# Kernel optimization log

Hardware: AMD Instinct MI355X
Metric: run time of the kernel (lower is better)

The kernel has to match this reference:

```python
import jax, jax.numpy as jnp
import numpy as np

D_MODEL = 1024
NUM_HEADS = 16
DEPTH = D_MODEL // NUM_HEADS
B, S = 4, 2048


def setup_inputs() -> dict:
    key = jax.random.key(0)
    ks = jax.random.split(key, 12)
    s = 1.0 / np.sqrt(D_MODEL)
    return {
        "q": jax.random.normal(ks[0], (B, S, D_MODEL), jnp.float32),
        "k": jax.random.normal(ks[1], (B, S, D_MODEL), jnp.float32),
        "v": jax.random.normal(ks[2], (B, S, D_MODEL), jnp.float32),
        "mask": jax.random.randint(ks[3], (B, S), 0, 2, jnp.int32),
        "wq_w": jax.random.uniform(ks[4], (D_MODEL, D_MODEL), jnp.float32, -s, s),
        "wq_b": jnp.zeros((D_MODEL,), jnp.float32),
        "wk_w": jax.random.uniform(ks[5], (D_MODEL, D_MODEL), jnp.float32, -s, s),
        "wk_b": jnp.zeros((D_MODEL,), jnp.float32),
        "wv_w": jax.random.uniform(ks[6], (D_MODEL, D_MODEL), jnp.float32, -s, s),
        "wv_b": jnp.zeros((D_MODEL,), jnp.float32),
        "wo_w": jax.random.uniform(ks[7], (D_MODEL, D_MODEL), jnp.float32, -s, s),
        "wo_b": jnp.zeros((D_MODEL,), jnp.float32),
    }


def _split_heads(x):
    # [B, S, D] -> [B, H, S, depth]
    b, s, _ = x.shape
    return x.reshape(b, s, NUM_HEADS, DEPTH).transpose(0, 2, 1, 3)


def reference(q, k, v, mask, wq_w, wq_b, wk_w, wk_b, wv_w, wv_b, wo_w, wo_b):
    qh = _split_heads(q @ wq_w.T + wq_b)
    kh = _split_heads(k @ wk_w.T + wk_b)
    vh = _split_heads(v @ wv_w.T + wv_b)
    # [B, H, Sq, Sk]
    logits = jnp.einsum("bhqd,bhkd->bhqk", qh, kh) / jnp.sqrt(
        jnp.asarray(DEPTH, jnp.float32))
    # 2D mask -> [B, 1, 1, Sk], masked_fill where mask == 0
    m = mask[:, None, None, :]
    logits = jnp.where(m == 0, jnp.asarray(-1e9, logits.dtype), logits)
    attn = jax.nn.softmax(logits, axis=-1)
    out = jnp.einsum("bhqk,bhkd->bhqd", attn, vh)
    out = out.transpose(0, 2, 1, 3).reshape(q.shape[0], -1, D_MODEL)
    return out @ wo_w.T + wo_b
```

## Files before the change

kernel.cpp:

```cpp
#include <hip/hip_runtime.h>
#include <hip/hip_bf16.h>
#include <stdint.h>

typedef __bf16 bf16_t;
typedef __bf16 bf16x8 __attribute__((ext_vector_type(8)));
typedef __bf16 bf16x2 __attribute__((ext_vector_type(2)));
typedef float  f32x4  __attribute__((ext_vector_type(4)));
typedef float  f32x16 __attribute__((ext_vector_type(16)));
typedef unsigned int u32;
typedef u32 u32x4 __attribute__((ext_vector_type(4)));

#define D_MODEL 1024
#define NHEAD   16
#define DEPTH   64
#define BATCH   4
#define SEQ     2048
#define MROWS   (BATCH*SEQ)

#define SC 0.18033688011112042f

__device__ __forceinline__ void gload16(const void* g, void* l) {
    __builtin_amdgcn_global_load_lds(
        (__attribute__((address_space(1))) void*)(uintptr_t)g,
        (__attribute__((address_space(3))) void*)l,
        16, 0, 0);
}

__device__ __forceinline__ u32 pk2(float a, float b) {
    bf16x2 t; t[0] = (bf16_t)a; t[1] = (bf16_t)b;
    return __builtin_bit_cast(u32, t);
}

__global__ __launch_bounds__(256) void cvt_kernel(const float* __restrict__ src,
                                                  bf16_t* __restrict__ dst, int n8) {
    int i = blockIdx.x * 256 + threadIdx.x;
    if (i >= n8) return;
    const float4* s4 = (const float4*)src;
    float4 a = s4[2*(size_t)i], b = s4[2*(size_t)i + 1];
    bf16x8 o;
    o[0] = (bf16_t)a.x; o[1] = (bf16_t)a.y; o[2] = (bf16_t)a.z; o[3] = (bf16_t)a.w;
    o[4] = (bf16_t)b.x; o[5] = (bf16_t)b.y; o[6] = (bf16_t)b.z; o[7] = (bf16_t)b.w;
    *(bf16x8*)(dst + 8*(size_t)i) = o;
}

__global__ __launch_bounds__(256) void vtrans_kernel(const bf16_t* __restrict__ Vp,
                                                     bf16_t* __restrict__ Vt) {
    __shared__ bf16_t T[64][257];
    const int bh = blockIdx.y;
    const int b = bh >> 4, h = bh & 15;
    const int s0 = blockIdx.x * 256;
    const int tid = threadIdx.x;
#pragma unroll
    for (int p = 0; p < 8; ++p) {
        int id = p*256 + tid;
        int sl = id >> 3, dg = id & 7;
        bf16x8 v = *(const bf16x8*)&Vp[((size_t)b*SEQ + s0 + sl)*D_MODEL + h*DEPTH + dg*8];
#pragma unroll
        for (int e = 0; e < 8; ++e) T[dg*8 + e][sl] = v[e];
    }
    __syncthreads();
#pragma unroll
    for (int p = 0; p < 8; ++p) {
        int id = p*256 + tid;
        int d = id >> 5, sg = id & 31;
        bf16x8 o;
#pragma unroll
        for (int e = 0; e < 8; ++e) {
            int sp = sg*8 + e;
            int s  = (sp & ~12) | ((sp & 4) << 1) | ((sp & 8) >> 1);
            o[e] = T[d][s];
        }
        *(bf16x8*)&Vt[((size_t)bh*DEPTH + d)*SEQ + s0 + sg*8] = o;
    }
}

template<int OUT_BF16>
__global__ __launch_bounds__(256) void gemm_bt(const bf16_t* __restrict__ A,
                                               const bf16_t* __restrict__ Bw,
                                               const float* __restrict__ bias,
                                               bf16_t* __restrict__ Cb,
                                               float* __restrict__ Cf,
                                               int M, int N, int K) {
    __shared__ bf16_t As[128*64];
    __shared__ bf16_t Bs[128*64];
    const int tid  = threadIdx.x;
    const int wave = tid >> 6, lane = tid & 63;
    const int lr = lane & 15, lk = (lane >> 4) * 8;
    const int bm = blockIdx.x * 128, bn = blockIdx.y * 128;
    const int wr = (wave >> 1) * 64, wc = (wave & 1) * 64;

    f32x4 acc[4][4] = {};

    for (int kt = 0; kt < K; kt += 64) {
#pragma unroll
        for (int p = 0; p < 4; ++p) {
            int chunk = p*256 + tid;
            int r  = chunk >> 3;
            int cs = ((chunk & 7) ^ (r & 7)) * 8;
            gload16(A  + (size_t)(bm + r)*K + kt + cs, As + (size_t)(p*256 + wave*64)*8);
            gload16(Bw + (size_t)(bn + r)*K + kt + cs, Bs + (size_t)(p*256 + wave*64)*8);
        }
        __syncthreads();
        const char* AsB = (const char*)As;
        const char* BsB = (const char*)Bs;
#pragma unroll
        for (int ks = 0; ks < 2; ++ks) {
            int kb = (ks*32 + lk) * 2;
            bf16x8 af[4], bfv[4];
#pragma unroll
            for (int mi = 0; mi < 4; ++mi) {
                int row = wr + mi*16 + lr;
                af[mi] = *(const bf16x8*)(AsB + ((row*128 + kb) ^ ((row & 7) << 4)));
            }
#pragma unroll
            for (int ni = 0; ni < 4; ++ni) {
                int row = wc + ni*16 + lr;
                bfv[ni] = *(const bf16x8*)(BsB + ((row*128 + kb) ^ ((row & 7) << 4)));
            }
            __builtin_amdgcn_s_setprio(1);
#pragma unroll
            for (int mi = 0; mi < 4; ++mi)
#pragma unroll
                for (int ni = 0; ni < 4; ++ni)
                    acc[mi][ni] = __builtin_amdgcn_mfma_f32_16x16x32_bf16(
                        af[mi], bfv[ni], acc[mi][ni], 0, 0, 0);
            __builtin_amdgcn_s_setprio(0);
        }
        __syncthreads();
    }

#pragma unroll
    for (int ni = 0; ni < 4; ++ni) {
        int col = bn + wc + ni*16 + lr;
        float bv = bias[col];
#pragma unroll
        for (int mi = 0; mi < 4; ++mi) {
#pragma unroll
            for (int j = 0; j < 4; ++j) {
                int row = bm + wr + mi*16 + (lane >> 4)*4 + j;
                float vv = acc[mi][ni][j] + bv;
                if (OUT_BF16) Cb[(size_t)row*N + col] = (bf16_t)vv;
                else          Cf[(size_t)row*N + col] = vv;
            }
        }
    }
}

__global__ __launch_bounds__(256) void attn_kernel(const bf16_t* __restrict__ Qp,
                                                   const bf16_t* __restrict__ Kp,
                                                   const bf16_t* __restrict__ Vt,
                                                   const int* __restrict__ mask,
                                                   bf16_t* __restrict__ AO) {
    __shared__ bf16_t Ks[2][64*64];
    __shared__ bf16_t Vs[2][64*64];
    __shared__ float  mb[2][64];

    const int tid  = threadIdx.x;
    const int wave = tid >> 6, lane = tid & 63;
    const int lr5 = lane & 31;
    const int hi  = lane >> 5;
    const int b = blockIdx.z, h = blockIdx.y, q0 = blockIdx.x * 128;
    const int qw = q0 + wave*32;
    const size_t base  = (size_t)b * SEQ * D_MODEL + (size_t)h * DEPTH;
    const size_t vbase = ((size_t)(b*NHEAD + h)) * DEPTH * SEQ;

    bf16x8 qf[4];
#pragma unroll
    for (int dc = 0; dc < 4; ++dc)
        qf[dc] = *(const bf16x8*)&Qp[base + (size_t)(qw + lr5)*D_MODEL + dc*16 + hi*8];

    f32x16 o0 = {}, o1 = {};
    float m_run = -1e30f, l_run = 0.f;

    {
#pragma unroll
        for (int p = 0; p < 2; ++p) {
            int chunk = p*256 + tid; int r = chunk >> 3;
            int cs = ((chunk & 7) ^ (r & 7)) * 8;
            gload16(Kp + base + (size_t)r*D_MODEL + cs, (bf16_t*)Ks[0] + (size_t)chunk*8);
            gload16(Vt + vbase + (size_t)r*SEQ + cs,   (bf16_t*)Vs[0] + (size_t)chunk*8);
        }
        if (tid < 64) mb[0][tid] = (mask[(size_t)b*SEQ + tid] == 0) ? -1e30f : 0.f;
    }
    __syncthreads();

    for (int t = 0; t < SEQ/64; ++t) {
        const int cur = t & 1, nxt = cur ^ 1;
        if (t + 1 < SEQ/64) {
#pragma unroll
            for (int p = 0; p < 2; ++p) {
                int chunk = p*256 + tid; int r = chunk >> 3;
                int cs = ((chunk & 7) ^ (r & 7)) * 8;
                gload16(Kp + base + (size_t)((t+1)*64 + r)*D_MODEL + cs,
                        (bf16_t*)Ks[nxt] + (size_t)chunk*8);
                gload16(Vt + vbase + (size_t)r*SEQ + (t+1)*64 + cs,
                        (bf16_t*)Vs[nxt] + (size_t)chunk*8);
            }
            if (tid < 64) mb[nxt][tid] = (mask[(size_t)b*SEQ + (t+1)*64 + tid] == 0) ? -1e30f : 0.f;
        }

        const char* KsB = (const char*)Ks[cur];
        f32x16 s0 = {}, s1 = {};
#pragma unroll
        for (int dc = 0; dc < 4; ++dc) {
            int colb = dc*32 + hi*16;
            int row0 = lr5, row1 = 32 + lr5;
            bf16x8 kf0 = *(const bf16x8*)(KsB + ((row0*128 + colb) ^ ((row0 & 7) << 4)));
            bf16x8 kf1 = *(const bf16x8*)(KsB + ((row1*128 + colb) ^ ((row1 & 7) << 4)));
            __builtin_amdgcn_s_setprio(1);
            s0 = __builtin_amdgcn_mfma_f32_32x32x16_bf16(kf0, qf[dc], s0, 0, 0, 0);
            s1 = __builtin_amdgcn_mfma_f32_32x32x16_bf16(kf1, qf[dc], s1, 0, 0, 0);
            __builtin_amdgcn_s_setprio(0);
        }

        const float* mbp = mb[cur];
        f32x4 mv[2][4];
#pragma unroll
        for (int kt = 0; kt < 2; ++kt)
#pragma unroll
            for (int g = 0; g < 4; ++g)
                mv[kt][g] = *(const f32x4*)&mbp[kt*32 + g*8 + hi*4];

        float pv[32];
#pragma unroll
        for (int r = 0; r < 16; ++r) {
            pv[r]      = s0[r]*SC + mv[0][r>>2][r&3];
            pv[16 + r] = s1[r]*SC + mv[1][r>>2][r&3];
        }

        float rmax = fmaxf(pv[0], pv[1]);
#pragma unroll
        for (int r = 2; r < 32; r += 2) rmax = fmaxf(fmaxf(pv[r], pv[r+1]), rmax);
        rmax = fmaxf(rmax, __shfl_xor(rmax, 32));

        if (!__all(rmax <= m_run + 8.f)) {
            float mn  = fmaxf(m_run, rmax);
            float fac = __builtin_exp2f(m_run - mn);
            m_run = mn;
            l_run *= fac;
#pragma unroll
            for (int r = 0; r < 16; ++r) { o0[r] *= fac; o1[r] *= fac; }
        }
        float sum = 0.f;
#pragma unroll
        for (int r = 0; r < 32; ++r) { pv[r] = __builtin_exp2f(pv[r] - m_run); sum += pv[r]; }
        sum += __shfl_xor(sum, 32);
        l_run += sum;

        const char* VsB = (const char*)Vs[cur];
#pragma unroll
        for (int kt = 0; kt < 2; ++kt) {
#pragma unroll
            for (int c = 0; c < 2; ++c) {
                u32x4 fwv;
#pragma unroll
                for (int i = 0; i < 4; ++i)
                    fwv[i] = pk2(pv[kt*16 + c*8 + 2*i], pv[kt*16 + c*8 + 2*i + 1]);
                bf16x8 pfrag = __builtin_bit_cast(bf16x8, fwv);
                int colb = kt*64 + c*32 + hi*16;
                int row0 = lr5, row1 = 32 + lr5;
                bf16x8 vf0 = *(const bf16x8*)(VsB + ((row0*128 + colb) ^ ((row0 & 7) << 4)));
                bf16x8 vf1 = *(const bf16x8*)(VsB + ((row1*128 + colb) ^ ((row1 & 7) << 4)));
                __builtin_amdgcn_s_setprio(1);
                o0 = __builtin_amdgcn_mfma_f32_32x32x16_bf16(vf0, pfrag, o0, 0, 0, 0);
                o1 = __builtin_amdgcn_mfma_f32_32x32x16_bf16(vf1, pfrag, o1, 0, 0, 0);
                __builtin_amdgcn_s_setprio(0);
            }
        }
        __syncthreads();
    }

    float inv = 1.f / l_run;
    char* TrB = (char*)Ks;
    const int qloc = wave*32 + lr5;
#pragma unroll
    for (int mt = 0; mt < 2; ++mt)
#pragma unroll
        for (int r = 0; r < 16; ++r) {
            int d = mt*32 + (r & 3) + 8*(r >> 2) + 4*hi;
            float val = (mt ? o1[r] : o0[r]) * inv;
            *(bf16_t*)(TrB + (qloc*128 + ((d*2) ^ ((qloc & 7) << 4)))) = (bf16_t)val;
        }
    __syncthreads();
#pragma unroll
    for (int p = 0; p < 4; ++p) {
        int id = p*256 + tid;
        int row = id >> 3, g = id & 7;
        bf16x8 v8 = *(const bf16x8*)(TrB + (row*128 + ((g*16) ^ ((row & 7) << 4))));
        *(bf16x8*)&AO[base + (size_t)(q0 + row)*D_MODEL + g*8] = v8;
    }
}

extern "C" void kernel_launch(void* const* d_in, const int* in_sizes, int n_in,
                              void* d_out, int out_size, void* d_ws, size_t ws_size,
                              hipStream_t stream) {
    (void)in_sizes; (void)n_in; (void)out_size; (void)ws_size;
    const float* q    = (const float*)d_in[0];
    const float* k    = (const float*)d_in[1];
    const float* v    = (const float*)d_in[2];
    const int*   mask = (const int*)d_in[3];
    const float* wq_w = (const float*)d_in[4];
    const float* wq_b = (const float*)d_in[5];
    const float* wk_w = (const float*)d_in[6];
    const float* wk_b = (const float*)d_in[7];
    const float* wv_w = (const float*)d_in[8];
    const float* wv_b = (const float*)d_in[9];
    const float* wo_w = (const float*)d_in[10];
    const float* wo_b = (const float*)d_in[11];
    float* out = (float*)d_out;

    const size_t ACT = (size_t)MROWS * D_MODEL;
    const size_t WSZ = (size_t)D_MODEL * D_MODEL;
    bf16_t* Xb = (bf16_t*)d_ws;
    bf16_t* Qp = Xb + ACT;
    bf16_t* Kp = Qp + ACT;
    bf16_t* Vp = Kp + ACT;
    bf16_t* Wq = Vp + ACT;
    bf16_t* Wk = Wq + WSZ;
    bf16_t* Wv = Wk + WSZ;
    bf16_t* Wo = Wv + WSZ;
    bf16_t* Vt = Xb;
    bf16_t* AO = Vp;

    const int wn8 = (int)(WSZ/8), an8 = (int)(ACT/8);
    cvt_kernel<<<dim3(wn8/256), dim3(256), 0, stream>>>(wq_w, Wq, wn8);
    cvt_kernel<<<dim3(wn8/256), dim3(256), 0, stream>>>(wk_w, Wk, wn8);
    cvt_kernel<<<dim3(wn8/256), dim3(256), 0, stream>>>(wv_w, Wv, wn8);
    cvt_kernel<<<dim3(wn8/256), dim3(256), 0, stream>>>(wo_w, Wo, wn8);

    dim3 ggrid(MROWS/128, D_MODEL/128);
    cvt_kernel<<<dim3(an8/256), dim3(256), 0, stream>>>(q, Xb, an8);
    gemm_bt<1><<<ggrid, dim3(256), 0, stream>>>(Xb, Wq, wq_b, Qp, nullptr, MROWS, D_MODEL, D_MODEL);
    cvt_kernel<<<dim3(an8/256), dim3(256), 0, stream>>>(k, Xb, an8);
    gemm_bt<1><<<ggrid, dim3(256), 0, stream>>>(Xb, Wk, wk_b, Kp, nullptr, MROWS, D_MODEL, D_MODEL);
    cvt_kernel<<<dim3(an8/256), dim3(256), 0, stream>>>(v, Xb, an8);
    gemm_bt<1><<<ggrid, dim3(256), 0, stream>>>(Xb, Wv, wv_b, Vp, nullptr, MROWS, D_MODEL, D_MODEL);

    vtrans_kernel<<<dim3(SEQ/256, NHEAD*BATCH), dim3(256), 0, stream>>>(Vp, Vt);

    attn_kernel<<<dim3(SEQ/128, NHEAD, BATCH), dim3(256), 0, stream>>>(Qp, Kp, Vt, mask, AO);

    gemm_bt<0><<<ggrid, dim3(256), 0, stream>>>(AO, Wo, wo_b, nullptr, out, MROWS, D_MODEL, D_MODEL);
}
```

Baseline: 285.4 us.

## Triple-buffer K/V tiles, preload mask bias once, and remap blocks across XCDs

Attention K/V staging moves from double to triple buffering, prefetching two tiles ahead. Each iteration waits with a partial vmcnt so loads can stay in flight across the barrier. The per-tile mask load is replaced by a single up-front conversion of the whole mask row into a bf16 bias array in shared memory. Blocks are remapped so each XCD handles consistent (batch, head) groups, which should improve L2 reuse of K/V. LDS usage rises, which may reduce occupancy, and the hand-written waitcnt depends on the exact count of outstanding loads.

```diff
diff --git a/kernel.cpp b/kernel.cpp
--- a/kernel.cpp
+++ b/kernel.cpp
@@ -4,6 +4,7 @@
 
 typedef __bf16 bf16_t;
 typedef __bf16 bf16x8 __attribute__((ext_vector_type(8)));
+typedef __bf16 bf16x4 __attribute__((ext_vector_type(4)));
 typedef __bf16 bf16x2 __attribute__((ext_vector_type(2)));
 typedef float  f32x4  __attribute__((ext_vector_type(4)));
 typedef float  f32x16 __attribute__((ext_vector_type(16)));
@@ -151,55 +152,73 @@
                                                    const bf16_t* __restrict__ Vt,
                                                    const int* __restrict__ mask,
                                                    bf16_t* __restrict__ AO) {
-    __shared__ bf16_t Ks[2][64*64];
-    __shared__ bf16_t Vs[2][64*64];
-    __shared__ float  mb[2][64];
+    __shared__ bf16_t Ks[3][64*64];
+    __shared__ bf16_t Vs[3][64*64];
+    __shared__ bf16_t mbias[SEQ];
 
     const int tid  = threadIdx.x;
     const int wave = tid >> 6, lane = tid & 63;
     const int lr5 = lane & 31;
     const int hi  = lane >> 5;
-    const int b = blockIdx.z, h = blockIdx.y, q0 = blockIdx.x * 128;
+
+    const int flat = blockIdx.x + 16*blockIdx.y + 256*blockIdx.z;
+    const int xcd = flat & 7, slot = flat >> 3;
+    const int bh = xcd + 8*(slot >> 4);
+    const int b = bh >> 4, h = bh & 15;
+    const int q0 = (slot & 15) * 128;
+
     const int qw = q0 + wave*32;
     const size_t base  = (size_t)b * SEQ * D_MODEL + (size_t)h * DEPTH;
-    const size_t vbase = ((size_t)(b*NHEAD + h)) * DEPTH * SEQ;
+    const size_t vbase = (size_t)bh * DEPTH * SEQ;
 
     bf16x8 qf[4];
 #pragma unroll
     for (int dc = 0; dc < 4; ++dc)
         qf[dc] = *(const bf16x8*)&Qp[base + (size_t)(qw + lr5)*D_MODEL + dc*16 + hi*8];
 
-    f32x16 o0 = {}, o1 = {};
-    float m_run = -1e30f, l_run = 0.f;
-
     {
+        const int4* mp = (const int4*)&mask[(size_t)b*SEQ + tid*8];
+        int4 m0 = mp[0], m1 = mp[1];
+        bf16x8 mm;
+        mm[0] = (m0.x == 0) ? (bf16_t)(-1e30f) : (bf16_t)0.0f;
+        mm[1] = (m0.y == 0) ? (bf16_t)(-1e30f) : (bf16_t)0.0f;
+        mm[2] = (m0.z == 0) ? (bf16_t)(-1e30f) : (bf16_t)0.0f;
+        mm[3] = (m0.w == 0) ? (bf16_t)(-1e30f) : (bf16_t)0.0f;
+        mm[4] = (m1.x == 0) ? (bf16_t)(-1e30f) : (bf16_t)0.0f;
+        mm[5] = (m1.y == 0) ? (bf16_t)(-1e30f) : (bf16_t)0.0f;
+        mm[6] = (m1.z == 0) ? (bf16_t)(-1e30f) : (bf16_t)0.0f;
+        mm[7] = (m1.w == 0) ? (bf16_t)(-1e30f) : (bf16_t)0.0f;
+        *(bf16x8*)&mbias[tid*8] = mm;
+    }
+
+    auto stage = [&](int t, int buf) {
 #pragma unroll
         for (int p = 0; p < 2; ++p) {
             int chunk = p*256 + tid; int r = chunk >> 3;
             int cs = ((chunk & 7) ^ (r & 7)) * 8;
-            gload16(Kp + base + (size_t)r*D_MODEL + cs, (bf16_t*)Ks[0] + (size_t)chunk*8);
-            gload16(Vt + vbase + (size_t)r*SEQ + cs,   (bf16_t*)Vs[0] + (size_t)chunk*8);
-        }
-        if (tid < 64) mb[0][tid] = (mask[(size_t)b*SEQ + tid] == 0) ? -1e30f : 0.f;
-    }
-    __syncthreads();
-
+            gload16(Kp + base + (size_t)(t*64 + r)*D_MODEL + cs,
+                    (bf16_t*)Ks[buf] + (size_t)chunk*8);
+            gload16(Vt + vbase + (size_t)r*SEQ + t*64 + cs,
+                    (bf16_t*)Vs[buf] + (size_t)chunk*8);
+        }
+    };
+
+    f32x16 o0 = {}, o1 = {};
+    float m_run = -1e30f, l_run = 0.f;
+
+    stage(0, 0);
+    stage(1, 1);
+    asm volatile("s_waitcnt vmcnt(4) lgkmcnt(0)");
+    __builtin_amdgcn_s_barrier();
+
+    int cb = 0;
     for (int t = 0; t < SEQ/64; ++t) {
-        const int cur = t & 1, nxt = cur ^ 1;
-        if (t + 1 < SEQ/64) {
-#pragma unroll
-            for (int p = 0; p < 2; ++p) {
-                int chunk = p*256 + tid; int r = chunk >> 3;
-                int cs = ((chunk & 7) ^ (r & 7)) * 8;
-                gload16(Kp + base + (size_t)((t+1)*64 + r)*D_MODEL + cs,
-                        (bf16_t*)Ks[nxt] + (size_t)chunk*8);
-                gload16(Vt + vbase + (size_t)r*SEQ + (t+1)*64 + cs,
-                        (bf16_t*)Vs[nxt] + (size_t)chunk*8);
-            }
-            if (tid < 64) mb[nxt][tid] = (mask[(size_t)b*SEQ + (t+1)*64 + tid] == 0) ? -1e30f : 0.f;
-        }
-
-        const char* KsB = (const char*)Ks[cur];
+        if (t + 2 < SEQ/64) {
+            int pb = cb + 2; if (pb >= 3) pb -= 3;
+            stage(t + 2, pb);
+        }
+
+        const char* KsB = (const char*)Ks[cb];
         f32x16 s0 = {}, s1 = {};
 #pragma unroll
         for (int dc = 0; dc < 4; ++dc) {
@@ -213,19 +232,21 @@
             __builtin_amdgcn_s_setprio(0);
         }
 
-        const float* mbp = mb[cur];
-        f32x4 mv[2][4];
+        float mvf[2][4][4];
 #pragma unroll
         for (int kt = 0; kt < 2; ++kt)
 #pragma unroll
-            for (int g = 0; g < 4; ++g)
-                mv[kt][g] = *(const f32x4*)&mbp[kt*32 + g*8 + hi*4];
+            for (int g = 0; g < 4; ++g) {
+                bf16x4 m4 = *(const bf16x4*)&mbias[t*64 + kt*32 + g*8 + hi*4];
+#pragma unroll
+                for (int e = 0; e < 4; ++e) mvf[kt][g][e] = (float)m4[e];
+            }
 
         float pv[32];
 #pragma unroll
         for (int r = 0; r < 16; ++r) {
-            pv[r]      = s0[r]*SC + mv[0][r>>2][r&3];
-            pv[16 + r] = s1[r]*SC + mv[1][r>>2][r&3];
+            pv[r]      = s0[r]*SC + mvf[0][r>>2][r&3];
+            pv[16 + r] = s1[r]*SC + mvf[1][r>>2][r&3];
         }
 
         float rmax = fmaxf(pv[0], pv[1]);
@@ -247,7 +268,7 @@
         sum += __shfl_xor(sum, 32);
         l_run += sum;
 
-        const char* VsB = (const char*)Vs[cur];
+        const char* VsB = (const char*)Vs[cb];
 #pragma unroll
         for (int kt = 0; kt < 2; ++kt) {
 #pragma unroll
@@ -267,7 +288,11 @@
                 __builtin_amdgcn_s_setprio(0);
             }
         }
-        __syncthreads();
+
+        if (t < SEQ/64 - 2) asm volatile("s_waitcnt vmcnt(4) lgkmcnt(0)");
+        else                asm volatile("s_waitcnt vmcnt(0) lgkmcnt(0)");
+        __builtin_amdgcn_s_barrier();
+        ++cb; if (cb == 3) cb = 0;
     }
 
     float inv = 1.f / l_run;
```

Measured after the change: 290.7 us. No clear change (+1.8%).
